# Optimization experiments

Measured on AMD Instinct MI355X. Metric: run time of the kernel, lower is better.

The kernel has to match this reference:

```python
import jax, jax.numpy as jnp
import numpy as np

LAMB_LABELS = 1.0
LAMB_BBOXES = 5.0
LAMB_GENIOU = 2.0


def box_cxcywh_to_xyxy(x):
    cx, cy, w, h = x[..., 0], x[..., 1], x[..., 2], x[..., 3]
    return jnp.stack([cx - 0.5 * w, cy - 0.5 * h, cx + 0.5 * w, cy + 0.5 * h], axis=-1)


def generalized_box_iou(b1, b2):
    # b1: [P,4] xyxy, b2: [T,4] xyxy -> [P,T] pairwise GIoU
    area1 = (b1[:, 2] - b1[:, 0]) * (b1[:, 3] - b1[:, 1])
    area2 = (b2[:, 2] - b2[:, 0]) * (b2[:, 3] - b2[:, 1])
    lt = jnp.maximum(b1[:, None, :2], b2[None, :, :2])
    rb = jnp.minimum(b1[:, None, 2:], b2[None, :, 2:])
    wh = jnp.clip(rb - lt, 0.0)
    inter = wh[..., 0] * wh[..., 1]
    union = area1[:, None] + area2[None, :] - inter
    iou = inter / union
    lt_e = jnp.minimum(b1[:, None, :2], b2[None, :, :2])
    rb_e = jnp.maximum(b1[:, None, 2:], b2[None, :, 2:])
    wh_e = jnp.clip(rb_e - lt_e, 0.0)
    area_e = wh_e[..., 0] * wh_e[..., 1]
    return iou - (area_e - union) / area_e


def setup_inputs() -> dict:
    key = jax.random.key(0)
    k1, k2, k3, k4 = jax.random.split(key, 4)
    B, N, C, T = 16, 900, 92, 960
    out_labels = jax.random.normal(k1, (B, N, C), dtype=jnp.float32)
    out_bboxes = jax.random.uniform(k2, (B, N, 4), dtype=jnp.float32)
    tgt_labels = jax.random.randint(k3, (T,), 0, C, dtype=jnp.int64)
    tgt_bboxes = jax.random.uniform(k4, (T, 4), dtype=jnp.float32)
    return {"out_labels": out_labels, "out_bboxes": out_bboxes,
            "tgt_labels": tgt_labels, "tgt_bboxes": tgt_bboxes}


def reference(out_labels, out_bboxes, tgt_labels, tgt_bboxes):
    B, N, C = out_labels.shape
    # '(b n) d' softmax over classes, then gather target-label columns
    probs = jax.nn.softmax(out_labels.reshape(B * N, C), axis=-1)
    cost_labels = 1.0 - probs[:, tgt_labels]                     # [BN, T]
    ob = out_bboxes.reshape(B * N, 4)
    # pairwise L1 (torch.cdist p=1)
    cost_bboxes = jnp.sum(jnp.abs(ob[:, None, :] - tgt_bboxes[None, :, :]), axis=-1)
    # NOTE: original converts only predicted boxes to xyxy (targets used as-is)
    cost_geniou = 1.0 - generalized_box_iou(box_cxcywh_to_xyxy(ob), tgt_bboxes)
    cost = (LAMB_LABELS * cost_labels + LAMB_BBOXES * cost_bboxes
            + LAMB_GENIOU * cost_geniou)
    return cost.reshape(B, N, -1)                                # [B, N, T]
```

## Files before the change

kernel.cpp:

```cpp
#include <hip/hip_runtime.h>
#include <math.h>

constexpr int kB = 16, kN = 900, kC = 92, kT = 960;
constexpr int kBN = kB * kN;
constexpr int ROWS = 4;
constexpr int THREADS = 256;

typedef float vf4 __attribute__((ext_vector_type(4)));

__global__ __launch_bounds__(THREADS) void matcher_kernel(
    const float* __restrict__ out_labels,
    const float* __restrict__ out_bboxes,
    const int*   __restrict__ tgt_labels,
    const float* __restrict__ tgt_bboxes,
    float*       __restrict__ cost)
{
    __shared__ float4 s_cl4[kC];
    __shared__ float4 s_rowA[ROWS];
    __shared__ float4 s_rowB[ROWS];
    __shared__ float  s_rowC[ROWS];

    const int tid  = threadIdx.x;
    const int row0 = blockIdx.x * ROWS;

    const int t0 = tid * 4;
    float4 tb[4]; float a2[4]; int4 lab;
    if (t0 < kT) {
        const float4* tb4 = (const float4*)tgt_bboxes;
        #pragma unroll
        for (int i = 0; i < 4; ++i) tb[i] = tb4[t0 + i];
        lab = ((const int4*)tgt_labels)[tid];
        #pragma unroll
        for (int i = 0; i < 4; ++i)
            a2[i] = (tb[i].z - tb[i].x) * (tb[i].w - tb[i].y);
    }

    {
        const int r = tid >> 6;
        const int lane = tid & 63;
        const int p = row0 + r;
        const float* lrow = out_labels + (size_t)p * kC;
        float x0 = (lane < kC)      ? lrow[lane]      : -INFINITY;
        float x1 = (lane + 64 < kC) ? lrow[lane + 64] : -INFINITY;
        float m = fmaxf(x0, x1);
        #pragma unroll
        for (int off = 32; off > 0; off >>= 1)
            m = fmaxf(m, __shfl_down(m, off, 64));
        m = __shfl(m, 0, 64);
        float e0 = (lane < kC)      ? __expf(x0 - m) : 0.0f;
        float e1 = (lane + 64 < kC) ? __expf(x1 - m) : 0.0f;
        float s = e0 + e1;
        #pragma unroll
        for (int off = 32; off > 0; off >>= 1)
            s += __shfl_down(s, off, 64);
        s = __shfl(s, 0, 64);
        float inv = 1.0f / s;
        float* clf = (float*)s_cl4;
        if (lane < kC)      clf[lane * 4 + r]        = 5.0f - e0 * inv;
        if (lane + 64 < kC) clf[(lane + 64) * 4 + r] = 5.0f - e1 * inv;
        if (lane == 0) {
            float4 bb = ((const float4*)out_bboxes)[p];
            float hw = 0.5f * bb.z, hh = 0.5f * bb.w;
            float bx0 = bb.x - hw, by0 = bb.y - hh;
            float bx1 = bb.x + hw, by1 = bb.y + hh;
            s_rowA[r] = bb;
            s_rowB[r] = make_float4(bx0, by0, bx1, by1);
            s_rowC[r] = (bx1 - bx0) * (by1 - by0);
        }
    }
    __syncthreads();

    if (t0 < kT) {
        float4 cls[4];
        cls[0] = s_cl4[lab.x];
        cls[1] = s_cl4[lab.y];
        cls[2] = s_cl4[lab.z];
        cls[3] = s_cl4[lab.w];
        #pragma unroll
        for (int r = 0; r < ROWS; ++r) {
            const int p = row0 + r;
            float4 ra = s_rowA[r];
            float4 rb = s_rowB[r];
            float area1 = s_rowC[r];
            vf4 res;
            #pragma unroll
            for (int i = 0; i < 4; ++i) {
                float4 t = tb[i];
                float l1 = fabsf(ra.x - t.x) + fabsf(ra.y - t.y)
                         + fabsf(ra.z - t.z) + fabsf(ra.w - t.w);
                float ltx = fmaxf(rb.x, t.x), lty = fmaxf(rb.y, t.y);
                float rbx = fminf(rb.z, t.z), rby = fminf(rb.w, t.w);
                float iw = fmaxf(rbx - ltx, 0.0f), ih = fmaxf(rby - lty, 0.0f);
                float inter = iw * ih;
                float uni = area1 + a2[i] - inter;
                float ex0 = fminf(rb.x, t.x), ey0 = fminf(rb.y, t.y);
                float ex1 = fmaxf(rb.z, t.z), ey1 = fmaxf(rb.w, t.w);
                float area_e = (ex1 - ex0) * (ey1 - ey0);
                float num = fmaf(uni, uni, inter * area_e);
                float rcp = __builtin_amdgcn_rcpf(uni * area_e);
                float v = (r == 0) ? cls[i].x : (r == 1) ? cls[i].y
                        : (r == 2) ? cls[i].z : cls[i].w;
                v = fmaf(5.0f, l1, v);
                v = fmaf(-2.0f * num, rcp, v);
                res[i] = v;
            }
            *((vf4*)(cost + (size_t)p * kT) + tid) = res;
        }
    }
}

extern "C" void kernel_launch(void* const* d_in, const int* in_sizes, int n_in,
                              void* d_out, int out_size, void* d_ws, size_t ws_size,
                              hipStream_t stream) {
    const float* out_labels = (const float*)d_in[0];
    const float* out_bboxes = (const float*)d_in[1];
    const int*   tgt_labels = (const int*)d_in[2];
    const float* tgt_bboxes = (const float*)d_in[3];
    float* cost = (float*)d_out;
    dim3 grid(kBN / ROWS);
    matcher_kernel<<<grid, THREADS, 0, stream>>>(out_labels, out_bboxes,
                                                 tgt_labels, tgt_bboxes, cost);
}
```

Measured before the change: 90.49 us.

## Process eight rows per block with two targets per thread

Each block now handles eight prediction rows with 512 threads instead of four rows with 256. Each thread covers two targets instead of four, so 480 of the 512 threads are active. Class costs are split across two shared tables of four rows each, and a launch-bounds occupancy hint is added. Stores become 8-byte vectors instead of 16-byte ones, which may reduce store efficiency, and 32 threads per block stay idle.

Result: no change. 89.62 us (-1.0%).

```diff
diff --git a/kernel.cpp b/kernel.cpp
--- a/kernel.cpp
+++ b/kernel.cpp
@@ -3,19 +3,20 @@
 
 constexpr int kB = 16, kN = 900, kC = 92, kT = 960;
 constexpr int kBN = kB * kN;
-constexpr int ROWS = 4;
-constexpr int THREADS = 256;
+constexpr int ROWS = 8;
+constexpr int THREADS = 512;
 
-typedef float vf4 __attribute__((ext_vector_type(4)));
+typedef float vf2 __attribute__((ext_vector_type(2)));
 
-__global__ __launch_bounds__(THREADS) void matcher_kernel(
+__global__ __launch_bounds__(THREADS, 6) void matcher_kernel(
     const float* __restrict__ out_labels,
     const float* __restrict__ out_bboxes,
     const int*   __restrict__ tgt_labels,
     const float* __restrict__ tgt_bboxes,
     float*       __restrict__ cost)
 {
-    __shared__ float4 s_cl4[kC];
+    __shared__ float4 s_clA[kC];
+    __shared__ float4 s_clB[kC];
     __shared__ float4 s_rowA[ROWS];
     __shared__ float4 s_rowB[ROWS];
     __shared__ float  s_rowC[ROWS];
@@ -23,16 +24,15 @@
     const int tid  = threadIdx.x;
     const int row0 = blockIdx.x * ROWS;
 
-    const int t0 = tid * 4;
-    float4 tb[4]; float a2[4]; int4 lab;
+    const int t0 = tid * 2;
+    float4 tb[2]; float a2[2]; int2 lab;
     if (t0 < kT) {
         const float4* tb4 = (const float4*)tgt_bboxes;
-        #pragma unroll
-        for (int i = 0; i < 4; ++i) tb[i] = tb4[t0 + i];
-        lab = ((const int4*)tgt_labels)[tid];
-        #pragma unroll
-        for (int i = 0; i < 4; ++i)
-            a2[i] = (tb[i].z - tb[i].x) * (tb[i].w - tb[i].y);
+        tb[0] = tb4[t0];
+        tb[1] = tb4[t0 + 1];
+        lab = ((const int2*)tgt_labels)[tid];
+        a2[0] = (tb[0].z - tb[0].x) * (tb[0].w - tb[0].y);
+        a2[1] = (tb[1].z - tb[1].x) * (tb[1].w - tb[1].y);
     }
 
     {
@@ -55,9 +55,10 @@
             s += __shfl_down(s, off, 64);
         s = __shfl(s, 0, 64);
         float inv = 1.0f / s;
-        float* clf = (float*)s_cl4;
-        if (lane < kC)      clf[lane * 4 + r]        = 5.0f - e0 * inv;
-        if (lane + 64 < kC) clf[(lane + 64) * 4 + r] = 5.0f - e1 * inv;
+        float* clf = (r < 4) ? (float*)s_clA : (float*)s_clB;
+        const int rr = r & 3;
+        if (lane < kC)      clf[lane * 4 + rr]        = 5.0f - e0 * inv;
+        if (lane + 64 < kC) clf[(lane + 64) * 4 + rr] = 5.0f - e1 * inv;
         if (lane == 0) {
             float4 bb = ((const float4*)out_bboxes)[p];
             float hw = 0.5f * bb.z, hh = 0.5f * bb.w;
@@ -71,20 +72,22 @@
     __syncthreads();
 
     if (t0 < kT) {
-        float4 cls[4];
-        cls[0] = s_cl4[lab.x];
-        cls[1] = s_cl4[lab.y];
-        cls[2] = s_cl4[lab.z];
-        cls[3] = s_cl4[lab.w];
+        float4 cls0 = s_clA[lab.x];
+        float4 cls1 = s_clA[lab.y];
         #pragma unroll
         for (int r = 0; r < ROWS; ++r) {
+            if (r == 4) {
+                cls0 = s_clB[lab.x];
+                cls1 = s_clB[lab.y];
+            }
             const int p = row0 + r;
             float4 ra = s_rowA[r];
             float4 rb = s_rowB[r];
             float area1 = s_rowC[r];
-            vf4 res;
+            const int rr = r & 3;
+            vf2 res;
             #pragma unroll
-            for (int i = 0; i < 4; ++i) {
+            for (int i = 0; i < 2; ++i) {
                 float4 t = tb[i];
                 float l1 = fabsf(ra.x - t.x) + fabsf(ra.y - t.y)
                          + fabsf(ra.z - t.z) + fabsf(ra.w - t.w);
@@ -98,13 +101,14 @@
                 float area_e = (ex1 - ex0) * (ey1 - ey0);
                 float num = fmaf(uni, uni, inter * area_e);
                 float rcp = __builtin_amdgcn_rcpf(uni * area_e);
-                float v = (r == 0) ? cls[i].x : (r == 1) ? cls[i].y
-                        : (r == 2) ? cls[i].z : cls[i].w;
+                float4 cls = i == 0 ? cls0 : cls1;
+                float v = (rr == 0) ? cls.x : (rr == 1) ? cls.y
+                        : (rr == 2) ? cls.z : cls.w;
                 v = fmaf(5.0f, l1, v);
                 v = fmaf(-2.0f * num, rcp, v);
                 res[i] = v;
             }
-            *((vf4*)(cost + (size_t)p * kT) + tid) = res;
+            *((vf2*)(cost + (size_t)p * kT + t0)) = res;
         }
     }
 }
```

## Map one wavefront per prediction row and drop block-wide barrier

Applied to the files above, without the earlier changes.

Each 64-lane wavefront now owns one prediction row. It computes that row's softmax with xor-shuffle reductions into a per-wave LDS slice, then loops over all 960 targets with scalar coalesced stores. This replaces the old design, where four rows shared a block with a __syncthreads and threads held four targets each with float4 stores. The intent is to remove the block barrier and the idle-thread imbalance. It also drops the max subtraction in the softmax and uses a hardware reciprocal. In exchange, target boxes, labels and target areas are reloaded and recomputed for every row, and large logits could overflow.

Measured after the change: 90.29 us. No clear change (-0.2%).

```diff
diff --git a/kernel.cpp b/kernel.cpp
--- a/kernel.cpp
+++ b/kernel.cpp
@@ -1,111 +1,68 @@
 #include <hip/hip_runtime.h>
 #include <math.h>
 
-constexpr int kB = 16, kN = 900, kC = 92, kT = 960;
-constexpr int kBN = kB * kN;
-constexpr int ROWS = 4;
-constexpr int THREADS = 256;
+constexpr int kC = 92, kT = 960;
+constexpr int kBN = 14400;
+constexpr int WPB = 8;
+constexpr int THREADS = WPB * 64;
 
-typedef float vf4 __attribute__((ext_vector_type(4)));
-
-__global__ __launch_bounds__(THREADS) void matcher_kernel(
+__global__ __launch_bounds__(THREADS, 6) void matcher_kernel(
     const float* __restrict__ out_labels,
     const float* __restrict__ out_bboxes,
     const int*   __restrict__ tgt_labels,
     const float* __restrict__ tgt_bboxes,
     float*       __restrict__ cost)
 {
-    __shared__ float4 s_cl4[kC];
-    __shared__ float4 s_rowA[ROWS];
-    __shared__ float4 s_rowB[ROWS];
-    __shared__ float  s_rowC[ROWS];
+    __shared__ float s_cls[WPB][96];
 
     const int tid  = threadIdx.x;
-    const int row0 = blockIdx.x * ROWS;
+    const int w    = tid >> 6;
+    const int lane = tid & 63;
+    const int p    = blockIdx.x * WPB + w;
 
-    const int t0 = tid * 4;
-    float4 tb[4]; float a2[4]; int4 lab;
-    if (t0 < kT) {
-        const float4* tb4 = (const float4*)tgt_bboxes;
-        #pragma unroll
-        for (int i = 0; i < 4; ++i) tb[i] = tb4[t0 + i];
-        lab = ((const int4*)tgt_labels)[tid];
-        #pragma unroll
-        for (int i = 0; i < 4; ++i)
-            a2[i] = (tb[i].z - tb[i].x) * (tb[i].w - tb[i].y);
-    }
+    const float* lrow = out_labels + (size_t)p * kC;
+    float e0 = __expf(lrow[lane]);
+    float e1 = (lane + 64 < kC) ? __expf(lrow[lane + 64]) : 0.0f;
+    float s = e0 + e1;
+    #pragma unroll
+    for (int m = 1; m < 64; m <<= 1)
+        s += __shfl_xor(s, m, 64);
+    float inv = __builtin_amdgcn_rcpf(s);
+    s_cls[w][lane] = fmaf(-e0, inv, 5.0f);
+    if (lane + 64 < kC) s_cls[w][lane + 64] = fmaf(-e1, inv, 5.0f);
 
-    {
-        const int r = tid >> 6;
-        const int lane = tid & 63;
-        const int p = row0 + r;
-        const float* lrow = out_labels + (size_t)p * kC;
-        float x0 = (lane < kC)      ? lrow[lane]      : -INFINITY;
-        float x1 = (lane + 64 < kC) ? lrow[lane + 64] : -INFINITY;
-        float m = fmaxf(x0, x1);
-        #pragma unroll
-        for (int off = 32; off > 0; off >>= 1)
-            m = fmaxf(m, __shfl_down(m, off, 64));
-        m = __shfl(m, 0, 64);
-        float e0 = (lane < kC)      ? __expf(x0 - m) : 0.0f;
-        float e1 = (lane + 64 < kC) ? __expf(x1 - m) : 0.0f;
-        float s = e0 + e1;
-        #pragma unroll
-        for (int off = 32; off > 0; off >>= 1)
-            s += __shfl_down(s, off, 64);
-        s = __shfl(s, 0, 64);
-        float inv = 1.0f / s;
-        float* clf = (float*)s_cl4;
-        if (lane < kC)      clf[lane * 4 + r]        = 5.0f - e0 * inv;
-        if (lane + 64 < kC) clf[(lane + 64) * 4 + r] = 5.0f - e1 * inv;
-        if (lane == 0) {
-            float4 bb = ((const float4*)out_bboxes)[p];
-            float hw = 0.5f * bb.z, hh = 0.5f * bb.w;
-            float bx0 = bb.x - hw, by0 = bb.y - hh;
-            float bx1 = bb.x + hw, by1 = bb.y + hh;
-            s_rowA[r] = bb;
-            s_rowB[r] = make_float4(bx0, by0, bx1, by1);
-            s_rowC[r] = (bx1 - bx0) * (by1 - by0);
-        }
-    }
-    __syncthreads();
+    float4 bb = ((const float4*)out_bboxes)[p];
+    float hw = 0.5f * bb.z, hh = 0.5f * bb.w;
+    float bx0 = bb.x - hw, by0 = bb.y - hh;
+    float bx1 = bb.x + hw, by1 = bb.y + hh;
+    float area1 = (bx1 - bx0) * (by1 - by0);
 
-    if (t0 < kT) {
-        float4 cls[4];
-        cls[0] = s_cl4[lab.x];
-        cls[1] = s_cl4[lab.y];
-        cls[2] = s_cl4[lab.z];
-        cls[3] = s_cl4[lab.w];
-        #pragma unroll
-        for (int r = 0; r < ROWS; ++r) {
-            const int p = row0 + r;
-            float4 ra = s_rowA[r];
-            float4 rb = s_rowB[r];
-            float area1 = s_rowC[r];
-            vf4 res;
-            #pragma unroll
-            for (int i = 0; i < 4; ++i) {
-                float4 t = tb[i];
-                float l1 = fabsf(ra.x - t.x) + fabsf(ra.y - t.y)
-                         + fabsf(ra.z - t.z) + fabsf(ra.w - t.w);
-                float ltx = fmaxf(rb.x, t.x), lty = fmaxf(rb.y, t.y);
-                float rbx = fminf(rb.z, t.z), rby = fminf(rb.w, t.w);
-                float iw = fmaxf(rbx - ltx, 0.0f), ih = fmaxf(rby - lty, 0.0f);
-                float inter = iw * ih;
-                float uni = area1 + a2[i] - inter;
-                float ex0 = fminf(rb.x, t.x), ey0 = fminf(rb.y, t.y);
-                float ex1 = fmaxf(rb.z, t.z), ey1 = fmaxf(rb.w, t.w);
-                float area_e = (ex1 - ex0) * (ey1 - ey0);
-                float num = fmaf(uni, uni, inter * area_e);
-                float rcp = __builtin_amdgcn_rcpf(uni * area_e);
-                float v = (r == 0) ? cls[i].x : (r == 1) ? cls[i].y
-                        : (r == 2) ? cls[i].z : cls[i].w;
-                v = fmaf(5.0f, l1, v);
-                v = fmaf(-2.0f * num, rcp, v);
-                res[i] = v;
-            }
-            *((vf4*)(cost + (size_t)p * kT) + tid) = res;
-        }
+    asm volatile("s_waitcnt lgkmcnt(0)" ::: "memory");
+
+    const float4* tb4 = (const float4*)tgt_bboxes;
+    float* crow = cost + (size_t)p * kT;
+    #pragma unroll 5
+    for (int k = 0; k < 15; ++k) {
+        const int t = lane + 64 * k;
+        float4 tbb = tb4[t];
+        int    lb  = tgt_labels[t];
+        float  cls = s_cls[w][lb];
+        float  a2  = (tbb.z - tbb.x) * (tbb.w - tbb.y);
+        float l1 = fabsf(bb.x - tbb.x) + fabsf(bb.y - tbb.y)
+                 + fabsf(bb.z - tbb.z) + fabsf(bb.w - tbb.w);
+        float ltx = fmaxf(bx0, tbb.x), lty = fmaxf(by0, tbb.y);
+        float rbx = fminf(bx1, tbb.z), rby = fminf(by1, tbb.w);
+        float iw = fmaxf(rbx - ltx, 0.0f), ih = fmaxf(rby - lty, 0.0f);
+        float inter = iw * ih;
+        float uni = area1 + a2 - inter;
+        float ex0 = fminf(bx0, tbb.x), ey0 = fminf(by0, tbb.y);
+        float ex1 = fmaxf(bx1, tbb.z), ey1 = fmaxf(by1, tbb.w);
+        float area_e = (ex1 - ex0) * (ey1 - ey0);
+        float num = fmaf(uni, uni, inter * area_e);
+        float rcp = __builtin_amdgcn_rcpf(uni * area_e);
+        float v = fmaf(5.0f, l1, cls);
+        v = fmaf(-2.0f * num, rcp, v);
+        crow[t] = v;
     }
 }
 
@@ -117,7 +74,7 @@
     const int*   tgt_labels = (const int*)d_in[2];
     const float* tgt_bboxes = (const float*)d_in[3];
     float* cost = (float*)d_out;
-    dim3 grid(kBN / ROWS);
+    dim3 grid(kBN / WPB);
     matcher_kernel<<<grid, THREADS, 0, stream>>>(out_labels, out_bboxes,
                                                  tgt_labels, tgt_bboxes, cost);
 }
```
